# Kernel optimization log

Measured on AMD Instinct MI355X. Metric: run time of the kernel, lower is better.

Reference implementation:

```python
import jax, jax.numpy as jnp
import numpy as np

N = 50000          # nodes
E = 800000         # edges (before self loops)
H = 4              # attention heads
C = 64             # per-head channels
D_IN = 256
NEG_ATT = 0.2      # GATConv attention LeakyReLU slope
NEG_ACT = 0.01     # nn.LeakyReLU default slope
EPS = 1e-5
MLP_DIMS = [64, 32, 16, 2]


def _gat_layer(x, src, dst, W, a_src, a_dst, b, concat):
    """PyG GATConv: gather -> segment-softmax over dst -> scatter-add."""
    n = x.shape[0]
    h = (x @ W).reshape(n, H, C)                       # [N,H,C]
    s = (h * a_src).sum(-1)                            # [N,H]
    d = (h * a_dst).sum(-1)                            # [N,H]
    e = jax.nn.leaky_relu(s[src] + d[dst], NEG_ATT)    # [E',H]
    m = jax.ops.segment_max(e, dst, num_segments=n)    # per-dst max (self loops -> no empty segs)
    w = jnp.exp(e - m[dst])
    den = jax.ops.segment_sum(w, dst, num_segments=n)
    alpha = w / den[dst]                               # [E',H]
    out = jax.ops.segment_sum(alpha[:, :, None] * h[src], dst, num_segments=n)  # [N,H,C]
    out = out.reshape(n, H * C) if concat else out.mean(axis=1)
    return out + b


def _graph_norm(x, w, b, a):
    mu = x.mean(axis=0, keepdims=True)
    y = x - a * mu
    var = (y * y).mean(axis=0, keepdims=True)
    return w * y * jax.lax.rsqrt(var + EPS) + b


def setup_inputs() -> dict:
    key = jax.random.key(0)
    ks = jax.random.split(key, 40)
    d = {
        'x': jax.random.normal(ks[0], (N, D_IN), dtype=jnp.float32),
        'edge_index': jax.random.randint(ks[1], (2, E), 0, N, dtype=jnp.int64),
    }
    dims_in = [D_IN, H * C, H * C]
    norm_dims = [H * C, H * C, C]
    k = 2
    for i in range(3):
        fan = dims_in[i]
        d[f'W{i}'] = jax.random.normal(ks[k], (fan, H * C), dtype=jnp.float32) / np.sqrt(fan); k += 1
        d[f'as{i}'] = jax.random.normal(ks[k], (H, C), dtype=jnp.float32) / np.sqrt(C); k += 1
        d[f'ad{i}'] = jax.random.normal(ks[k], (H, C), dtype=jnp.float32) / np.sqrt(C); k += 1
        d[f'b{i}'] = jnp.zeros((norm_dims[i],), dtype=jnp.float32)
        d[f'gw{i}'] = jnp.ones((norm_dims[i],), dtype=jnp.float32)
        d[f'gb{i}'] = jnp.zeros((norm_dims[i],), dtype=jnp.float32)
        d[f'ga{i}'] = jnp.ones((norm_dims[i],), dtype=jnp.float32)
    for j in range(3):
        fi, fo = MLP_DIMS[j], MLP_DIMS[j + 1]
        d[f'mW{j}'] = jax.random.normal(ks[k], (fi, fo), dtype=jnp.float32) / np.sqrt(fi); k += 1
        d[f'mb{j}'] = jnp.zeros((fo,), dtype=jnp.float32)
    return d


def reference(x, edge_index,
              W0, as0, ad0, b0, gw0, gb0, ga0,
              W1, as1, ad1, b1, gw1, gb1, ga1,
              W2, as2, ad2, b2, gw2, gb2, ga2,
              mW0, mb0, mW1, mb1, mW2, mb2):
    n = x.shape[0]
    loop = jnp.arange(n, dtype=edge_index.dtype)
    src = jnp.concatenate([edge_index[0], loop])   # add self loops (PyG default)
    dst = jnp.concatenate([edge_index[1], loop])

    h = _gat_layer(x, src, dst, W0, as0, ad0, b0, concat=True)
    h = jax.nn.leaky_relu(_graph_norm(h, gw0, gb0, ga0), NEG_ACT)
    h = _gat_layer(h, src, dst, W1, as1, ad1, b1, concat=True)
    h = jax.nn.leaky_relu(_graph_norm(h, gw1, gb1, ga1), NEG_ACT)
    h = _gat_layer(h, src, dst, W2, as2, ad2, b2, concat=False)
    h = jax.nn.leaky_relu(_graph_norm(h, gw2, gb2, ga2), NEG_ACT)

    h = jax.nn.relu(h @ mW0 + mb0)
    h = jax.nn.relu(h @ mW1 + mb1)
    return h @ mW2 + mb2
```

## Files before the change

kernel.cpp:

```cpp
#include <hip/hip_runtime.h>

#define NN 50000
#define EE 800000
#define ET 850000
#define HH 4
#define CC 64
#define FDIM 256

#define SCAN_BLK 512
#define SCAN_NB ((NN + SCAN_BLK - 1) / SCAN_BLK)

typedef unsigned short ushort;
typedef __bf16 bf16x8 __attribute__((ext_vector_type(8)));
typedef float floatx4 __attribute__((ext_vector_type(4)));
typedef ushort ushort8v __attribute__((ext_vector_type(8)));
struct ushort4s { ushort x, y, z, w; };

__device__ __forceinline__ ushort f2bf(float f) {
  union { float f; unsigned u; } v; v.f = f;
  unsigned r = v.u + 0x7fffu + ((v.u >> 16) & 1u);
  return (ushort)(r >> 16);
}
__device__ __forceinline__ float bf2f(ushort u) {
  return __uint_as_float(((unsigned)u) << 16);
}

__device__ __forceinline__ int get_edge(const void* p, int is64, long long idx) {
  if (is64) return (int)((const long long*)p)[idx];
  return ((const int*)p)[idx];
}

__global__ void detect_kernel(const unsigned int* p, int* flag) {
  __shared__ unsigned red[256];
  int t = threadIdx.x;
  unsigned o = 0;
  for (int i = 0; i < 4; i++) o |= p[(t * 4 + i) * 2 + 1];
  red[t] = o;
  __syncthreads();
  for (int s = 128; s > 0; s >>= 1) {
    if (t < s) red[t] |= red[t + s];
    __syncthreads();
  }
  if (t == 0) *flag = (red[0] == 0) ? 1 : 0;
}

__global__ void degree_kernel(const void* eidx, const int* flag, int* deg) {
  int k = blockIdx.x * blockDim.x + threadIdx.x;
  if (k >= ET) return;
  int is64 = *flag;
  int dst = (k < EE) ? get_edge(eidx, is64, (long long)EE + k) : (k - EE);
  atomicAdd(&deg[dst], 1);
}

__global__ __launch_bounds__(SCAN_BLK) void scan1_kernel(const int* __restrict__ deg,
                                                         int* __restrict__ rowptr,
                                                         int* __restrict__ bsum) {
  __shared__ int sm[SCAN_BLK];
  int t = threadIdx.x;
  int i = blockIdx.x * SCAN_BLK + t;
  int v = (i < NN) ? deg[i] : 0;
  sm[t] = v;
  __syncthreads();
#pragma unroll
  for (int o = 1; o < SCAN_BLK; o <<= 1) {
    int u = (t >= o) ? sm[t - o] : 0;
    __syncthreads();
    sm[t] += u;
    __syncthreads();
  }
  if (i < NN) rowptr[i] = sm[t] - v;
  if (t == SCAN_BLK - 1) bsum[blockIdx.x] = sm[t];
}

__global__ __launch_bounds__(128) void scan2_kernel(const int* __restrict__ bsum,
                                                    int* __restrict__ boff,
                                                    int* __restrict__ rowptr) {
  __shared__ int sm[128];
  int t = threadIdx.x;
  int v = (t < SCAN_NB) ? bsum[t] : 0;
  sm[t] = v;
  __syncthreads();
#pragma unroll
  for (int o = 1; o < 128; o <<= 1) {
    int u = (t >= o) ? sm[t - o] : 0;
    __syncthreads();
    sm[t] += u;
    __syncthreads();
  }
  if (t < SCAN_NB) boff[t] = sm[t] - v;
  if (t == 0) rowptr[NN] = ET;
}

__global__ __launch_bounds__(SCAN_BLK) void scan3_kernel(int* __restrict__ rowptr,
                                                         int* __restrict__ cursor,
                                                         const int* __restrict__ boff) {
  int i = blockIdx.x * SCAN_BLK + threadIdx.x;
  if (i >= NN) return;
  int v = rowptr[i] + boff[blockIdx.x];
  rowptr[i] = v;
  cursor[i] = v;
}

__global__ void fill_kernel(const void* eidx, const int* flag, int* cursor, int* csr_src) {
  int k = blockIdx.x * blockDim.x + threadIdx.x;
  if (k >= ET) return;
  int is64 = *flag;
  int src, dst;
  if (k < EE) {
    src = get_edge(eidx, is64, k);
    dst = get_edge(eidx, is64, (long long)EE + k);
  } else {
    src = dst = k - EE;
  }
  int pos = atomicAdd(&cursor[dst], 1);
  csr_src[pos] = src;
}

__global__ void conv_x_kernel(const float* __restrict__ x, ushort* __restrict__ xb) {
  int i = blockIdx.x * 256 + threadIdx.x;
  float4 v = ((const float4*)x)[i];
  ushort4s o;
  o.x = f2bf(v.x); o.y = f2bf(v.y); o.z = f2bf(v.z); o.w = f2bf(v.w);
  ((ushort4s*)xb)[i] = o;
}

__global__ void conv_w_kernel(const float* __restrict__ W, ushort* __restrict__ Wt) {
  int idx = blockIdx.x * 256 + threadIdx.x;
  int k = idx >> 8, n = idx & 255;
  Wt[n * 256 + k] = f2bf(W[idx]);
}

__global__ __launch_bounds__(256) void gemm_bf16(const ushort* __restrict__ A,
                                                 const ushort* __restrict__ Bt,
                                                 ushort* __restrict__ C) {
  __shared__ ushort As[8 * 512];
  __shared__ ushort Bs[8 * 512];
  int tid = threadIdx.x, w = tid >> 6, l = tid & 63;
  int brow0 = blockIdx.x * 128, bcol0 = blockIdx.y * 128;
  int lm = l & 15, lk = (l >> 4) * 8;
  int s0 = 2 * w, s1 = 2 * w + 1;
  int ar0 = min(brow0 + s0 * 16 + lm, NN - 1);
  int ar1 = min(brow0 + s1 * 16 + lm, NN - 1);
  const ushort* ag0 = A + (size_t)ar0 * 256 + lk;
  const ushort* ag1 = A + (size_t)ar1 * 256 + lk;
  const ushort* bg0 = Bt + (size_t)(bcol0 + s0 * 16 + lm) * 256 + lk;
  const ushort* bg1 = Bt + (size_t)(bcol0 + s1 * 16 + lm) * 256 + lk;

  floatx4 acc[4][4];
#pragma unroll
  for (int i = 0; i < 4; i++)
#pragma unroll
    for (int j = 0; j < 4; j++) acc[i][j] = floatx4{0.f, 0.f, 0.f, 0.f};

  int wm = (w >> 1) * 4, wn = (w & 1) * 4;

  for (int k0 = 0; k0 < 256; k0 += 32) {
    ushort8v a0 = *(const ushort8v*)(ag0 + k0);
    ushort8v a1 = *(const ushort8v*)(ag1 + k0);
    ushort8v b0 = *(const ushort8v*)(bg0 + k0);
    ushort8v b1 = *(const ushort8v*)(bg1 + k0);
    *(ushort8v*)&As[s0 * 512 + l * 8] = a0;
    *(ushort8v*)&As[s1 * 512 + l * 8] = a1;
    *(ushort8v*)&Bs[s0 * 512 + l * 8] = b0;
    *(ushort8v*)&Bs[s1 * 512 + l * 8] = b1;
    __syncthreads();
    bf16x8 af[4], bfr[4];
#pragma unroll
    for (int i = 0; i < 4; i++) af[i] = *(const bf16x8*)&As[(wm + i) * 512 + l * 8];
#pragma unroll
    for (int j = 0; j < 4; j++) bfr[j] = *(const bf16x8*)&Bs[(wn + j) * 512 + l * 8];
#pragma unroll
    for (int i = 0; i < 4; i++)
#pragma unroll
      for (int j = 0; j < 4; j++)
        acc[i][j] = __builtin_amdgcn_mfma_f32_16x16x32_bf16(af[i], bfr[j], acc[i][j], 0, 0, 0);
    __syncthreads();
  }

  int quad = l >> 4;
#pragma unroll
  for (int i = 0; i < 4; i++) {
    int r0 = brow0 + (wm + i) * 16 + quad * 4;
#pragma unroll
    for (int j = 0; j < 4; j++) {
      int col = bcol0 + (wn + j) * 16 + lm;
#pragma unroll
      for (int r = 0; r < 4; r++) {
        int row = r0 + r;
        if (row < NN) C[(size_t)row * 256 + col] = f2bf(acc[i][j][r]);
      }
    }
  }
}

__global__ __launch_bounds__(256) void sd_kernel(const ushort* __restrict__ h,
                                                 const float* __restrict__ as_,
                                                 const float* __restrict__ ad_,
                                                 float* __restrict__ s, float* __restrict__ d) {
  int w = threadIdx.x >> 6;
  int l = threadIdx.x & 63;
  int n = blockIdx.x * 4 + w;
  ushort4s hv = *(const ushort4s*)(h + (size_t)n * FDIM + l * 4);
  float4 av = ((const float4*)as_)[l];
  float4 dv = ((const float4*)ad_)[l];
  float f0 = bf2f(hv.x), f1 = bf2f(hv.y), f2 = bf2f(hv.z), f3 = bf2f(hv.w);
  float ps = f0 * av.x + f1 * av.y + f2 * av.z + f3 * av.w;
  float pd = f0 * dv.x + f1 * dv.y + f2 * dv.z + f3 * dv.w;
#pragma unroll
  for (int o = 1; o < 16; o <<= 1) {
    ps += __shfl_xor(ps, o);
    pd += __shfl_xor(pd, o);
  }
  if ((l & 15) == 0) {
    s[n * HH + (l >> 4)] = ps;
    d[n * HH + (l >> 4)] = pd;
  }
}

template <bool CONCAT>
__global__ __launch_bounds__(256) void agg_kernel(const ushort* __restrict__ hb,
                                                  const float* __restrict__ s_arr,
                                                  const float* __restrict__ d_arr,
                                                  const int* __restrict__ rowptr,
                                                  const int* __restrict__ csr_src,
                                                  const float* __restrict__ bias,
                                                  void* __restrict__ outp) {
  int w = __builtin_amdgcn_readfirstlane(threadIdx.x >> 6);
  int l = threadIdx.x & 63;
  int head = l >> 4;
  int n = blockIdx.x * 4 + w;
  int beg = rowptr[n], end = rowptr[n + 1];
  float dh = d_arr[n * HH + head];
  float a0 = 0.f, a1 = 0.f, a2 = 0.f, a3 = 0.f, den = 0.f;

  int i = beg;
  for (; i + 4 <= end; i += 4) {
    int s0 = csr_src[i], s1 = csr_src[i + 1], s2 = csr_src[i + 2], s3 = csr_src[i + 3];
    float e0 = s_arr[s0 * HH + head] + dh;
    float e1 = s_arr[s1 * HH + head] + dh;
    float e2 = s_arr[s2 * HH + head] + dh;
    float e3 = s_arr[s3 * HH + head] + dh;
    ushort4s h0 = *(const ushort4s*)(hb + (unsigned)(s0 * FDIM + l * 4));
    ushort4s h1 = *(const ushort4s*)(hb + (unsigned)(s1 * FDIM + l * 4));
    ushort4s h2 = *(const ushort4s*)(hb + (unsigned)(s2 * FDIM + l * 4));
    ushort4s h3 = *(const ushort4s*)(hb + (unsigned)(s3 * FDIM + l * 4));
    e0 = (e0 > 0.f) ? e0 : 0.2f * e0;  float w0 = __expf(e0);
    e1 = (e1 > 0.f) ? e1 : 0.2f * e1;  float w1 = __expf(e1);
    e2 = (e2 > 0.f) ? e2 : 0.2f * e2;  float w2 = __expf(e2);
    e3 = (e3 > 0.f) ? e3 : 0.2f * e3;  float w3 = __expf(e3);
    den += (w0 + w1) + (w2 + w3);
    a0 = fmaf(w0, bf2f(h0.x), a0); a1 = fmaf(w0, bf2f(h0.y), a1);
    a2 = fmaf(w0, bf2f(h0.z), a2); a3 = fmaf(w0, bf2f(h0.w), a3);
    a0 = fmaf(w1, bf2f(h1.x), a0); a1 = fmaf(w1, bf2f(h1.y), a1);
    a2 = fmaf(w1, bf2f(h1.z), a2); a3 = fmaf(w1, bf2f(h1.w), a3);
    a0 = fmaf(w2, bf2f(h2.x), a0); a1 = fmaf(w2, bf2f(h2.y), a1);
    a2 = fmaf(w2, bf2f(h2.z), a2); a3 = fmaf(w2, bf2f(h2.w), a3);
    a0 = fmaf(w3, bf2f(h3.x), a0); a1 = fmaf(w3, bf2f(h3.y), a1);
    a2 = fmaf(w3, bf2f(h3.z), a2); a3 = fmaf(w3, bf2f(h3.w), a3);
  }
  for (; i < end; i++) {
    int s0 = csr_src[i];
    float e0 = s_arr[s0 * HH + head] + dh;
    ushort4s h0 = *(const ushort4s*)(hb + (unsigned)(s0 * FDIM + l * 4));
    e0 = (e0 > 0.f) ? e0 : 0.2f * e0;
    float w0 = __expf(e0);
    den += w0;
    a0 = fmaf(w0, bf2f(h0.x), a0); a1 = fmaf(w0, bf2f(h0.y), a1);
    a2 = fmaf(w0, bf2f(h0.z), a2); a3 = fmaf(w0, bf2f(h0.w), a3);
  }
  float inv = 1.0f / den;
  float r0 = a0 * inv, r1 = a1 * inv, r2 = a2 * inv, r3 = a3 * inv;

  if (CONCAT) {
    float4 bv = ((const float4*)bias)[l];
    ushort4s o;
    o.x = f2bf(r0 + bv.x); o.y = f2bf(r1 + bv.y);
    o.z = f2bf(r2 + bv.z); o.w = f2bf(r3 + bv.w);
    ((ushort4s*)outp)[(unsigned)(n * 64 + l)] = o;
  } else {
    r0 += __shfl_xor(r0, 16); r1 += __shfl_xor(r1, 16);
    r2 += __shfl_xor(r2, 16); r3 += __shfl_xor(r3, 16);
    r0 += __shfl_xor(r0, 32); r1 += __shfl_xor(r1, 32);
    r2 += __shfl_xor(r2, 32); r3 += __shfl_xor(r3, 32);
    if (l < 16) {
      float4 bv = ((const float4*)bias)[l];
      float4 o;
      o.x = 0.25f * r0 + bv.x; o.y = 0.25f * r1 + bv.y;
      o.z = 0.25f * r2 + bv.z; o.w = 0.25f * r3 + bv.w;
      ((float4*)outp)[(unsigned)(n * 16 + l)] = o;
    }
  }
}

__global__ __launch_bounds__(256) void norm_reduce_bf(const ushort* __restrict__ xin,
                                                      float* colsum, float* colsumsq) {
  int f = threadIdx.x;
  int r0 = blockIdx.x * 128;
  int r1 = min(NN, r0 + 128);
  float s1 = 0.f, s2 = 0.f;
  for (int r = r0; r < r1; r++) {
    float v = bf2f(xin[(size_t)r * FDIM + f]);
    s1 += v; s2 += v * v;
  }
  atomicAdd(&colsum[f], s1);
  atomicAdd(&colsumsq[f], s2);
}

__global__ __launch_bounds__(256) void norm_reduce_f32(const float* __restrict__ xin,
                                                       float* colsum, float* colsumsq) {
  int f = threadIdx.x & (CC - 1);
  int rl = threadIdx.x / CC;
  int r0 = blockIdx.x * 128;
  int r1 = min(NN, r0 + 128);
  float s1 = 0.f, s2 = 0.f;
  for (int r = r0 + rl; r < r1; r += 4) {
    float v = xin[(size_t)r * CC + f];
    s1 += v; s2 += v * v;
  }
  atomicAdd(&colsum[f], s1);
  atomicAdd(&colsumsq[f], s2);
}

__global__ __launch_bounds__(256) void norm_apply_bf(const ushort* __restrict__ in,
                                                     ushort* __restrict__ outb,
                                                     const float* __restrict__ colsum,
                                                     const float* __restrict__ colsumsq,
                                                     const float* __restrict__ ga,
                                                     const float* __restrict__ gw,
                                                     const float* __restrict__ gb) {
  __shared__ float sc[FDIM], sh[FDIM];
  int t = threadIdx.x;
  {
    const float invn = 1.0f / (float)NN;
    float mu = colsum[t] * invn;
    float ex2 = colsumsq[t] * invn;
    float a = ga[t];
    float var = fmaxf(ex2 - (2.f * a - a * a) * mu * mu, 0.f);
    float s = gw[t] * rsqrtf(var + 1e-5f);
    sc[t] = s; sh[t] = gb[t] - s * a * mu;
  }
  __syncthreads();
  const int total = NN * FDIM / 4;
  for (int i = blockIdx.x * 256 + t; i < total; i += gridDim.x * 256) {
    int f0 = (i * 4) & (FDIM - 1);
    ushort4s v = ((const ushort4s*)in)[i];
    float y0 = sc[f0 + 0] * bf2f(v.x) + sh[f0 + 0];
    float y1 = sc[f0 + 1] * bf2f(v.y) + sh[f0 + 1];
    float y2 = sc[f0 + 2] * bf2f(v.z) + sh[f0 + 2];
    float y3 = sc[f0 + 3] * bf2f(v.w) + sh[f0 + 3];
    ushort4s o;
    o.x = f2bf((y0 > 0.f) ? y0 : 0.01f * y0);
    o.y = f2bf((y1 > 0.f) ? y1 : 0.01f * y1);
    o.z = f2bf((y2 > 0.f) ? y2 : 0.01f * y2);
    o.w = f2bf((y3 > 0.f) ? y3 : 0.01f * y3);
    ((ushort4s*)outb)[i] = o;
  }
}

__global__ __launch_bounds__(256) void norm_apply_f32(float* __restrict__ xio,
                                                      const float* __restrict__ colsum,
                                                      const float* __restrict__ colsumsq,
                                                      const float* __restrict__ ga,
                                                      const float* __restrict__ gw,
                                                      const float* __restrict__ gb) {
  __shared__ float sc[CC], sh[CC];
  int t = threadIdx.x;
  if (t < CC) {
    const float invn = 1.0f / (float)NN;
    float mu = colsum[t] * invn;
    float ex2 = colsumsq[t] * invn;
    float a = ga[t];
    float var = fmaxf(ex2 - (2.f * a - a * a) * mu * mu, 0.f);
    float s = gw[t] * rsqrtf(var + 1e-5f);
    sc[t] = s; sh[t] = gb[t] - s * a * mu;
  }
  __syncthreads();
  const int total = NN * CC;
  for (int i = blockIdx.x * 256 + t; i < total; i += gridDim.x * 256) {
    int f = i & (CC - 1);
    float y = sc[f] * xio[i] + sh[f];
    xio[i] = (y > 0.f) ? y : 0.01f * y;
  }
}

__global__ __launch_bounds__(256) void mlp_kernel(const float* __restrict__ xin,
                                                  const float* mW0, const float* mb0,
                                                  const float* mW1, const float* mb1,
                                                  const float* mW2, const float* mb2,
                                                  float* __restrict__ out) {
  __shared__ float W0s[64 * 32];
  __shared__ float W1s[32 * 16];
  __shared__ float W2s[16 * 2];
  __shared__ float b0s[32], b1s[16], b2s[2];
  int t = threadIdx.x;
  for (int i = t; i < 2048; i += 256) W0s[i] = mW0[i];
  for (int i = t; i < 512; i += 256) W1s[i] = mW1[i];
  if (t < 32) { W2s[t] = mW2[t]; b0s[t] = mb0[t]; }
  if (t < 16) b1s[t] = mb1[t];
  if (t < 2) b2s[t] = mb2[t];
  __syncthreads();
  int node = blockIdx.x * 256 + t;
  if (node >= NN) return;
  float in[64];
  const float* xr = xin + (size_t)node * 64;
#pragma unroll
  for (int k = 0; k < 64; k++) in[k] = xr[k];
  float h1[32];
#pragma unroll
  for (int j = 0; j < 32; j++) h1[j] = b0s[j];
#pragma unroll
  for (int k = 0; k < 64; k++) {
    float v = in[k];
#pragma unroll
    for (int j = 0; j < 32; j++) h1[j] += v * W0s[k * 32 + j];
  }
#pragma unroll
  for (int j = 0; j < 32; j++) h1[j] = fmaxf(h1[j], 0.f);
  float h2[16];
#pragma unroll
  for (int j = 0; j < 16; j++) h2[j] = b1s[j];
#pragma unroll
  for (int k = 0; k < 32; k++) {
    float v = h1[k];
#pragma unroll
    for (int j = 0; j < 16; j++) h2[j] += v * W1s[k * 16 + j];
  }
#pragma unroll
  for (int j = 0; j < 16; j++) h2[j] = fmaxf(h2[j], 0.f);
  float o0 = b2s[0], o1 = b2s[1];
#pragma unroll
  for (int k = 0; k < 16; k++) {
    o0 += h2[k] * W2s[k * 2 + 0];
    o1 += h2[k] * W2s[k * 2 + 1];
  }
  out[(size_t)node * 2 + 0] = o0;
  out[(size_t)node * 2 + 1] = o1;
}

extern "C" void kernel_launch(void* const* d_in, const int* in_sizes, int n_in,
                              void* d_out, int out_size, void* d_ws, size_t ws_size,
                              hipStream_t stream) {
  const float* x = (const float*)d_in[0];
  const void* ei = d_in[1];
  const float* W[3]   = {(const float*)d_in[2],  (const float*)d_in[9],  (const float*)d_in[16]};
  const float* as_[3] = {(const float*)d_in[3],  (const float*)d_in[10], (const float*)d_in[17]};
  const float* ad_[3] = {(const float*)d_in[4],  (const float*)d_in[11], (const float*)d_in[18]};
  const float* b_[3]  = {(const float*)d_in[5],  (const float*)d_in[12], (const float*)d_in[19]};
  const float* gw[3]  = {(const float*)d_in[6],  (const float*)d_in[13], (const float*)d_in[20]};
  const float* gb[3]  = {(const float*)d_in[7],  (const float*)d_in[14], (const float*)d_in[21]};
  const float* ga[3]  = {(const float*)d_in[8],  (const float*)d_in[15], (const float*)d_in[22]};
  const float* mW0 = (const float*)d_in[23];
  const float* mb0 = (const float*)d_in[24];
  const float* mW1 = (const float*)d_in[25];
  const float* mb1 = (const float*)d_in[26];
  const float* mW2 = (const float*)d_in[27];
  const float* mb2 = (const float*)d_in[28];
  float* out = (float*)d_out;

  char* ws = (char*)d_ws;
  size_t off = 0;
  auto take = [&](size_t bytes) -> char* {
    char* p = ws + off;
    off = (off + bytes + 255) & ~(size_t)255;
    return p;
  };
  ushort* xb    = (ushort*)take((size_t)NN * FDIM * 2);
  ushort* hb    = (ushort*)take((size_t)NN * FDIM * 2);
  ushort* yb    = (ushort*)take((size_t)NN * FDIM * 2);
  ushort* aggb  = (ushort*)take((size_t)NN * FDIM * 2);
  float* bufD   = (float*)take((size_t)NN * CC * 4);
  ushort* Wt[3];
  for (int i = 0; i < 3; i++) Wt[i] = (ushort*)take((size_t)256 * 256 * 2);
  float* s_arr  = (float*)take((size_t)NN * HH * 4);
  float* d_arr  = (float*)take((size_t)NN * HH * 4);
  int* deg      = (int*)take((size_t)NN * 4);
  int* cursor   = (int*)take((size_t)NN * 4);
  int* rowptr   = (int*)take((size_t)(NN + 1) * 4);
  int* csr_src  = (int*)take((size_t)ET * 4);
  int* bsum     = (int*)take(512);
  int* boff     = (int*)take(512);
  float* colsum   = (float*)take(1024);
  float* colsumsq = (float*)take(1024);
  int* flag       = (int*)take(256);

  hipMemsetAsync(deg, 0, (size_t)NN * 4, stream);
  detect_kernel<<<1, 256, 0, stream>>>((const unsigned int*)ei, flag);
  degree_kernel<<<(ET + 255) / 256, 256, 0, stream>>>(ei, flag, deg);
  scan1_kernel<<<SCAN_NB, SCAN_BLK, 0, stream>>>(deg, rowptr, bsum);
  scan2_kernel<<<1, 128, 0, stream>>>(bsum, boff, rowptr);
  scan3_kernel<<<SCAN_NB, SCAN_BLK, 0, stream>>>(rowptr, cursor, boff);
  fill_kernel<<<(ET + 255) / 256, 256, 0, stream>>>(ei, flag, cursor, csr_src);

  conv_x_kernel<<<(NN * FDIM / 4 + 255) / 256, 256, 0, stream>>>(x, xb);
  for (int L = 0; L < 3; L++)
    conv_w_kernel<<<256, 256, 0, stream>>>(W[L], Wt[L]);

  const ushort* lin = xb;
  for (int L = 0; L < 3; L++) {
    gemm_bf16<<<dim3((NN + 127) / 128, 2), 256, 0, stream>>>(lin, Wt[L], hb);
    sd_kernel<<<NN / 4, 256, 0, stream>>>(hb, as_[L], ad_[L], s_arr, d_arr);
    hipMemsetAsync(colsum, 0, 2048, stream);
    if (L < 2) {
      agg_kernel<true><<<NN / 4, 256, 0, stream>>>(hb, s_arr, d_arr, rowptr, csr_src, b_[L], aggb);
      norm_reduce_bf<<<(NN + 127) / 128, 256, 0, stream>>>(aggb, colsum, colsumsq);
      norm_apply_bf<<<1024, 256, 0, stream>>>(aggb, yb, colsum, colsumsq, ga[L], gw[L], gb[L]);
      lin = yb;
    } else {
      agg_kernel<false><<<NN / 4, 256, 0, stream>>>(hb, s_arr, d_arr, rowptr, csr_src, b_[L], bufD);
      norm_reduce_f32<<<(NN + 127) / 128, 256, 0, stream>>>(bufD, colsum, colsumsq);
      norm_apply_f32<<<512, 256, 0, stream>>>(bufD, colsum, colsumsq, ga[L], gw[L], gb[L]);
    }
  }
  mlp_kernel<<<(NN + 255) / 256, 256, 0, stream>>>(bufD, mW0, mb0, mW1, mb1, mW2, mb2, out);
}
```

Measured before the change: 714.3 us.

## Fuse attention scores into GEMM epilogue, fold final norm into MLP, batch weight conversion

The attention source and destination dot products are now computed from the GEMM accumulators in the epilogue and reduced across lanes, then atomically added into zeroed s/d arrays. This removes the separate sd_kernel pass that re-read h. The final GraphNorm apply step is folded into the MLP input load, removing one read-write pass over the f32 buffer. The three weight conversions are merged into one launch with a 2D grid. In exchange the change adds float atomics, which make summation order nondeterministic, plus a wider memset per layer. The s/d values are also now computed from fp32 accumulators rather than the bf16-rounded h.

```diff
diff --git a/kernel.cpp b/kernel.cpp
--- a/kernel.cpp
+++ b/kernel.cpp
@@ -124,7 +124,12 @@
   ((ushort4s*)xb)[i] = o;
 }
 
-__global__ void conv_w_kernel(const float* __restrict__ W, ushort* __restrict__ Wt) {
+__global__ void conv_w_kernel(const float* __restrict__ W0, const float* __restrict__ W1,
+                              const float* __restrict__ W2,
+                              ushort* __restrict__ T0, ushort* __restrict__ T1,
+                              ushort* __restrict__ T2) {
+  const float* W = (blockIdx.y == 0) ? W0 : (blockIdx.y == 1) ? W1 : W2;
+  ushort* Wt = (blockIdx.y == 0) ? T0 : (blockIdx.y == 1) ? T1 : T2;
   int idx = blockIdx.x * 256 + threadIdx.x;
   int k = idx >> 8, n = idx & 255;
   Wt[n * 256 + k] = f2bf(W[idx]);
@@ -132,7 +137,11 @@
 
 __global__ __launch_bounds__(256) void gemm_bf16(const ushort* __restrict__ A,
                                                  const ushort* __restrict__ Bt,
-                                                 ushort* __restrict__ C) {
+                                                 ushort* __restrict__ C,
+                                                 const float* __restrict__ as_,
+                                                 const float* __restrict__ ad_,
+                                                 float* __restrict__ s_arr,
+                                                 float* __restrict__ d_arr) {
   __shared__ ushort As[8 * 512];
   __shared__ ushort Bs[8 * 512];
   int tid = threadIdx.x, w = tid >> 6, l = tid & 63;
@@ -191,29 +200,34 @@
       }
     }
   }
-}
-
-__global__ __launch_bounds__(256) void sd_kernel(const ushort* __restrict__ h,
-                                                 const float* __restrict__ as_,
-                                                 const float* __restrict__ ad_,
-                                                 float* __restrict__ s, float* __restrict__ d) {
-  int w = threadIdx.x >> 6;
-  int l = threadIdx.x & 63;
-  int n = blockIdx.x * 4 + w;
-  ushort4s hv = *(const ushort4s*)(h + (size_t)n * FDIM + l * 4);
-  float4 av = ((const float4*)as_)[l];
-  float4 dv = ((const float4*)ad_)[l];
-  float f0 = bf2f(hv.x), f1 = bf2f(hv.y), f2 = bf2f(hv.z), f3 = bf2f(hv.w);
-  float ps = f0 * av.x + f1 * av.y + f2 * av.z + f3 * av.w;
-  float pd = f0 * dv.x + f1 * dv.y + f2 * dv.z + f3 * dv.w;
-#pragma unroll
-  for (int o = 1; o < 16; o <<= 1) {
-    ps += __shfl_xor(ps, o);
-    pd += __shfl_xor(pd, o);
-  }
-  if ((l & 15) == 0) {
-    s[n * HH + (l >> 4)] = ps;
-    d[n * HH + (l >> 4)] = pd;
+  float asv[4], adv[4];
+#pragma unroll
+  for (int j = 0; j < 4; j++) {
+    int col = bcol0 + (wn + j) * 16 + lm;
+    asv[j] = as_[col];
+    adv[j] = ad_[col];
+  }
+  int head = (bcol0 >> 6) + (wn >> 2);
+#pragma unroll
+  for (int i = 0; i < 4; i++) {
+#pragma unroll
+    for (int r = 0; r < 4; r++) {
+      float sp = acc[i][0][r] * asv[0] + acc[i][1][r] * asv[1] +
+                 acc[i][2][r] * asv[2] + acc[i][3][r] * asv[3];
+      float dp = acc[i][0][r] * adv[0] + acc[i][1][r] * adv[1] +
+                 acc[i][2][r] * adv[2] + acc[i][3][r] * adv[3];
+      sp += __shfl_xor(sp, 1); dp += __shfl_xor(dp, 1);
+      sp += __shfl_xor(sp, 2); dp += __shfl_xor(dp, 2);
+      sp += __shfl_xor(sp, 4); dp += __shfl_xor(dp, 4);
+      sp += __shfl_xor(sp, 8); dp += __shfl_xor(dp, 8);
+      if (lm == 0) {
+        int row = brow0 + (wm + i) * 16 + quad * 4 + r;
+        if (row < NN) {
+          atomicAdd(&s_arr[row * HH + head], sp);
+          atomicAdd(&d_arr[row * HH + head], dp);
+        }
+      }
+    }
   }
 }
 
@@ -357,14 +371,27 @@
   }
 }
 
-__global__ __launch_bounds__(256) void norm_apply_f32(float* __restrict__ xio,
-                                                      const float* __restrict__ colsum,
-                                                      const float* __restrict__ colsumsq,
-                                                      const float* __restrict__ ga,
-                                                      const float* __restrict__ gw,
-                                                      const float* __restrict__ gb) {
+__global__ __launch_bounds__(256) void mlp_kernel(const float* __restrict__ xin,
+                                                  const float* __restrict__ colsum,
+                                                  const float* __restrict__ colsumsq,
+                                                  const float* __restrict__ ga,
+                                                  const float* __restrict__ gw,
+                                                  const float* __restrict__ gb,
+                                                  const float* mW0, const float* mb0,
+                                                  const float* mW1, const float* mb1,
+                                                  const float* mW2, const float* mb2,
+                                                  float* __restrict__ out) {
+  __shared__ float W0s[64 * 32];
+  __shared__ float W1s[32 * 16];
+  __shared__ float W2s[16 * 2];
+  __shared__ float b0s[32], b1s[16], b2s[2];
   __shared__ float sc[CC], sh[CC];
   int t = threadIdx.x;
+  for (int i = t; i < 2048; i += 256) W0s[i] = mW0[i];
+  for (int i = t; i < 512; i += 256) W1s[i] = mW1[i];
+  if (t < 32) { W2s[t] = mW2[t]; b0s[t] = mb0[t]; }
+  if (t < 16) b1s[t] = mb1[t];
+  if (t < 2) b2s[t] = mb2[t];
   if (t < CC) {
     const float invn = 1.0f / (float)NN;
     float mu = colsum[t] * invn;
@@ -375,36 +402,15 @@
     sc[t] = s; sh[t] = gb[t] - s * a * mu;
   }
   __syncthreads();
-  const int total = NN * CC;
-  for (int i = blockIdx.x * 256 + t; i < total; i += gridDim.x * 256) {
-    int f = i & (CC - 1);
-    float y = sc[f] * xio[i] + sh[f];
-    xio[i] = (y > 0.f) ? y : 0.01f * y;
-  }
-}
-
-__global__ __launch_bounds__(256) void mlp_kernel(const float* __restrict__ xin,
-                                                  const float* mW0, const float* mb0,
-                                                  const float* mW1, const float* mb1,
-                                                  const float* mW2, const float* mb2,
-                                                  float* __restrict__ out) {
-  __shared__ float W0s[64 * 32];
-  __shared__ float W1s[32 * 16];
-  __shared__ float W2s[16 * 2];
-  __shared__ float b0s[32], b1s[16], b2s[2];
-  int t = threadIdx.x;
-  for (int i = t; i < 2048; i += 256) W0s[i] = mW0[i];
-  for (int i = t; i < 512; i += 256) W1s[i] = mW1[i];
-  if (t < 32) { W2s[t] = mW2[t]; b0s[t] = mb0[t]; }
-  if (t < 16) b1s[t] = mb1[t];
-  if (t < 2) b2s[t] = mb2[t];
-  __syncthreads();
   int node = blockIdx.x * 256 + t;
   if (node >= NN) return;
   float in[64];
   const float* xr = xin + (size_t)node * 64;
 #pragma unroll
-  for (int k = 0; k < 64; k++) in[k] = xr[k];
+  for (int k = 0; k < 64; k++) {
+    float y = sc[k] * xr[k] + sh[k];
+    in[k] = (y > 0.f) ? y : 0.01f * y;
+  }
   float h1[32];
 #pragma unroll
   for (int j = 0; j < 32; j++) h1[j] = b0s[j];
@@ -473,15 +479,16 @@
   for (int i = 0; i < 3; i++) Wt[i] = (ushort*)take((size_t)256 * 256 * 2);
   float* s_arr  = (float*)take((size_t)NN * HH * 4);
   float* d_arr  = (float*)take((size_t)NN * HH * 4);
+  float* colsum   = (float*)take(1024);
+  float* colsumsq = (float*)take(1024);
+  const size_t zero_bytes = (size_t)NN * HH * 4 * 2 + 2048;
   int* deg      = (int*)take((size_t)NN * 4);
   int* cursor   = (int*)take((size_t)NN * 4);
   int* rowptr   = (int*)take((size_t)(NN + 1) * 4);
   int* csr_src  = (int*)take((size_t)ET * 4);
   int* bsum     = (int*)take(512);
   int* boff     = (int*)take(512);
-  float* colsum   = (float*)take(1024);
-  float* colsumsq = (float*)take(1024);
-  int* flag       = (int*)take(256);
+  int* flag     = (int*)take(256);
 
   hipMemsetAsync(deg, 0, (size_t)NN * 4, stream);
   detect_kernel<<<1, 256, 0, stream>>>((const unsigned int*)ei, flag);
@@ -492,14 +499,13 @@
   fill_kernel<<<(ET + 255) / 256, 256, 0, stream>>>(ei, flag, cursor, csr_src);
 
   conv_x_kernel<<<(NN * FDIM / 4 + 255) / 256, 256, 0, stream>>>(x, xb);
-  for (int L = 0; L < 3; L++)
-    conv_w_kernel<<<256, 256, 0, stream>>>(W[L], Wt[L]);
+  conv_w_kernel<<<dim3(256, 3), 256, 0, stream>>>(W[0], W[1], W[2], Wt[0], Wt[1], Wt[2]);
 
   const ushort* lin = xb;
   for (int L = 0; L < 3; L++) {
-    gemm_bf16<<<dim3((NN + 127) / 128, 2), 256, 0, stream>>>(lin, Wt[L], hb);
-    sd_kernel<<<NN / 4, 256, 0, stream>>>(hb, as_[L], ad_[L], s_arr, d_arr);
-    hipMemsetAsync(colsum, 0, 2048, stream);
+    hipMemsetAsync(s_arr, 0, zero_bytes, stream);
+    gemm_bf16<<<dim3((NN + 127) / 128, 2), 256, 0, stream>>>(lin, Wt[L], hb,
+                                                             as_[L], ad_[L], s_arr, d_arr);
     if (L < 2) {
       agg_kernel<true><<<NN / 4, 256, 0, stream>>>(hb, s_arr, d_arr, rowptr, csr_src, b_[L], aggb);
       norm_reduce_bf<<<(NN + 127) / 128, 256, 0, stream>>>(aggb, colsum, colsumsq);
@@ -508,8 +514,9 @@
     } else {
       agg_kernel<false><<<NN / 4, 256, 0, stream>>>(hb, s_arr, d_arr, rowptr, csr_src, b_[L], bufD);
       norm_reduce_f32<<<(NN + 127) / 128, 256, 0, stream>>>(bufD, colsum, colsumsq);
-      norm_apply_f32<<<512, 256, 0, stream>>>(bufD, colsum, colsumsq, ga[L], gw[L], gb[L]);
     }
   }
-  mlp_kernel<<<(NN + 255) / 256, 256, 0, stream>>>(bufD, mW0, mb0, mW1, mb1, mW2, mb2, out);
-}
+  mlp_kernel<<<(NN + 255) / 256, 256, 0, stream>>>(bufD, colsum, colsumsq,
+                                                   ga[2], gw[2], gb[2],
+                                                   mW0, mb0, mW1, mb1, mW2, mb2, out);
+}
```

Result: slower. 733.6 us (+2.7%).
